# Performance work log

Measured on AMD Instinct MI355X. Metric: run time of the kernel, lower is better.

The kernel has to match this reference:

```python
import jax, jax.numpy as jnp
import numpy as np

B, H, N = 2, 4, 8192
K = 32       # sub_size
TEMP = 2.0   # temperature for the soft permutation indicator


def setup_inputs() -> dict:
    key = jax.random.key(0)
    ranking = jax.random.normal(key, (B, H, N, 1), dtype=jnp.float32)
    return {"ranking": ranking, "i": 0, "j": N}


@jax.custom_vjp
def hsigmoid(x):
    # Hard step indicator (x > 0) with straight-through gradient (CoCN Hsigmoid)
    return (x > 0).astype(x.dtype)

def _hs_fwd(x):
    return hsigmoid(x), None

def _hs_bwd(res, g):
    return (g,)

hsigmoid.defvjp(_hs_fwd, _hs_bwd)


def _windows(x, n, k):
    # circular pad last dim by k-1, then unfold into sliding windows of size k
    xp = jnp.concatenate([x, x[..., :k - 1]], axis=-1)
    idx = jnp.arange(n)[:, None] + jnp.arange(k)[None, :]   # (n, k)
    return xp[..., idx]                                      # (..., n, k)


def reference(ranking, i, j):
    b, h, n = ranking.shape[:3]
    k = K
    r = ranking[..., 0]                                      # (b,h,n)
    order = jnp.argsort(r, axis=2, stable=True)              # (b,h,n) stable sort indices
    r_sorted = jnp.take_along_axis(r, order, axis=2)

    val_win = _windows(r_sorted, n, k)                       # (b,h,n,k)
    idx_win = _windows(order.astype(jnp.float32), n, k).astype(jnp.int32)

    # scatter windows back to original node order == gather by inverse permutation
    inv = jnp.argsort(order, axis=2)                         # (b,h,n)
    val_win = jnp.take_along_axis(val_win, inv[..., None], axis=2)
    idx_win = jnp.take_along_axis(idx_win, inv[..., None], axis=2)

    # within each window, sort by original node index (stable), reorder values alike
    k_order = jnp.argsort(idx_win, axis=-1, stable=True)
    sorted_idx = jnp.take_along_axis(idx_win, k_order, axis=-1)
    val_win = jnp.take_along_axis(val_win, k_order, axis=-1)

    # slice node window [i, i+j)
    val_win = val_win[:, :, i:i + j]                         # (b,h,j,k)
    sorted_idx = sorted_idx[:, :, i:i + j]

    # (b,j,h,k) -> (b*j, h, k, 1)
    x = jnp.transpose(val_win, (0, 2, 1, 3)).reshape(-1, h, k, 1)
    rel = x - jnp.swapaxes(x, -1, -2)                        # (b*j,h,k,k)
    tie_bias = jnp.triu((rel == 0).astype(jnp.float32), 1)   # break ties above diagonal
    rel = rel + tie_bias
    uni = hsigmoid(jax.nn.relu(rel))                         # 1 where strictly greater
    rank = jnp.sum(uni, axis=-2, keepdims=True)              # (b*j,h,1,k)

    ind = jnp.arange(k, dtype=jnp.float32)[:, None] - rank   # (b*j,h,k,k)
    ind = jnp.where(ind < 0, ind + k, ind)
    perm = jnp.exp(-ind * TEMP)
    return perm, sorted_idx
```

## Files before the change

kernel.cpp:

```cpp
#include <hip/hip_runtime.h>
#include <stdint.h>

#define B_ 2
#define H_ 4
#define N_ 8192
#define K_ 32
#define ROWS 8
#define NTOT (ROWS * N_)
#define PERM_ELEMS ((size_t)B_ * N_ * H_ * K_ * K_)

__global__ __launch_bounds__(256) void pack_keys(const float* __restrict__ ranking,
                                                 uint64_t* __restrict__ keys,
                                                 int* __restrict__ rank) {
    const int g = blockIdx.x * 256 + threadIdx.x;
    uint32_t u = __float_as_uint(ranking[g]);
    u = (u & 0x80000000u) ? ~u : (u | 0x80000000u);
    keys[g] = ((uint64_t)u << 13) | (uint32_t)(g & (N_ - 1));
    rank[g] = 0;
}

#define JT 1024
#define IT 2048
#define EPT 8

__global__ __launch_bounds__(256) void rank_count(const uint64_t* __restrict__ keys,
                                                  int* __restrict__ rank) {
    __shared__ uint64_t jk[JT];
    const int blk = blockIdx.x;
    const int jt  = blk & 7;
    const int it  = (blk >> 3) & 3;
    const int row = blk >> 5;
    const uint64_t* rk = keys + (size_t)row * N_;

    for (int j = threadIdx.x; j < JT; j += 256)
        jk[j] = rk[jt * JT + j];

    uint64_t my[EPT];
    const int ibase = it * IT + threadIdx.x;
    #pragma unroll
    for (int e = 0; e < EPT; ++e) my[e] = rk[ibase + e * 256];
    __syncthreads();

    int cnt[EPT] = {0, 0, 0, 0, 0, 0, 0, 0};
    for (int j = 0; j < JT; j += 2) {
        const uint64_t k0 = jk[j];
        const uint64_t k1 = jk[j + 1];
        #pragma unroll
        for (int e = 0; e < EPT; ++e) {
            cnt[e] += (k0 < my[e]);
            cnt[e] += (k1 < my[e]);
        }
    }
    #pragma unroll
    for (int e = 0; e < EPT; ++e)
        atomicAdd(&rank[(size_t)row * N_ + ibase + e * 256], cnt[e]);
}

__global__ __launch_bounds__(256) void scatter_sorted(const float* __restrict__ ranking,
                                                      const int* __restrict__ rank,
                                                      int2* __restrict__ vid,
                                                      int* __restrict__ inv) {
    const int g = blockIdx.x * 256 + threadIdx.x;
    const int row = g >> 13;
    const int s = rank[g];
    inv[g] = s;
    vid[(size_t)row * N_ + s] = make_int2(__float_as_int(ranking[g]), g & (N_ - 1));
}

__global__ __launch_bounds__(256) void windows_kernel(
    const int2* __restrict__ vid,
    const int* __restrict__ inv,
    float* __restrict__ perm_out,
    float* __restrict__ idx_out)
{
    __shared__ float etabN[K_];
    __shared__ float etabP[K_];
    __shared__ uint64_t wk[8][K_];
    __shared__ float2 cinfo[8][K_ + 1];
    __shared__ float idf[8][K_];

    const int tid = threadIdx.x;
    if (tid < K_) {
        etabN[tid] = expf(-2.0f * (float)tid);
        etabP[tid] = expf(2.0f * (float)tid);
    }

    const int wave = tid >> 6;
    const int lane = tid & 63;
    const int half = lane >> 5;
    const int m    = lane & 31;
    const int ws   = wave * 2 + half;

    const int w   = blockIdx.x * 8 + ws;
    const int row = w >> 13;
    const int n   = w & (N_ - 1);

    const int t = inv[(size_t)row * N_ + n];
    int g = t + m; if (g >= N_) g -= N_;
    const int2 vi = vid[(size_t)row * N_ + g];
    const int id = vi.y;
    uint32_t u = (uint32_t)vi.x;
    u = (u & 0x80000000u) ? ~u : (u | 0x80000000u);
    const int rid = (N_ - 1) - id;
    const uint64_t key2 = ((uint64_t)u << 13) | (uint32_t)rid;

    wk[ws][m] = key2;
    __syncthreads();

    int rank = 0, pos = 0;
    #pragma unroll
    for (int p = 0; p < K_; ++p) {
        const uint64_t kp = wk[ws][p];
        rank += (kp > key2);
        pos  += ((int)((uint32_t)kp & (uint32_t)(N_ - 1)) > rid);
    }

    cinfo[ws][pos] = make_float2(etabP[rank], __int_as_float(rank));
    idf[ws][pos]   = (float)id;
    __syncthreads();

    idx_out[((size_t)row * N_ + n) * K_ + m] = idf[ws][m];

    const int b = row >> 2;
    const int h = row & 3;
    float4* pout = (float4*)(perm_out + (((size_t)b * N_ + n) * H_ + h) * (K_ * K_));
    const float E64C = 1.6038108e-28f;

    #pragma unroll
    for (int q = 0; q < 8; ++q) {
        const int f4 = q * 32 + m;
        const int mm = f4 >> 3;
        const int j0 = (f4 & 7) * 4;
        const float a = etabN[mm];
        const float2 c0 = cinfo[ws][j0 + 0];
        const float2 c1 = cinfo[ws][j0 + 1];
        const float2 c2 = cinfo[ws][j0 + 2];
        const float2 c3 = cinfo[ws][j0 + 3];
        float4 val;
        val.x = a * c0.x * (mm < __float_as_int(c0.y) ? E64C : 1.0f);
        val.y = a * c1.x * (mm < __float_as_int(c1.y) ? E64C : 1.0f);
        val.z = a * c2.x * (mm < __float_as_int(c2.y) ? E64C : 1.0f);
        val.w = a * c3.x * (mm < __float_as_int(c3.y) ? E64C : 1.0f);
        pout[f4] = val;
    }
}

extern "C" void kernel_launch(void* const* d_in, const int* in_sizes, int n_in,
                              void* d_out, int out_size, void* d_ws, size_t ws_size,
                              hipStream_t stream) {
    const float* ranking = (const float*)d_in[0];

    char* ws = (char*)d_ws;
    uint64_t* keys = (uint64_t*)ws;
    int*      rank = (int*)(ws + 512 * 1024);
    int2*     vid  = (int2*)(ws + 768 * 1024);
    int*      inv  = (int*)(ws + 1280 * 1024);

    float* perm_out = (float*)d_out;
    float* idx_out  = perm_out + PERM_ELEMS;

    hipLaunchKernelGGL(pack_keys, dim3(NTOT / 256), dim3(256), 0, stream,
                       ranking, keys, rank);
    hipLaunchKernelGGL(rank_count, dim3(256), dim3(256), 0, stream,
                       keys, rank);
    hipLaunchKernelGGL(scatter_sorted, dim3(NTOT / 256), dim3(256), 0, stream,
                       ranking, rank, vid, inv);
    hipLaunchKernelGGL(windows_kernel, dim3((ROWS * N_) / 8), dim3(256), 0, stream,
                       vid, inv, perm_out, idx_out);
}
```

Measured before the change: 318.2 us.

## Fuse rank counting with scatter and hoist window-loop loads

Merges the tiled rank-count kernel (which used atomics) and the scatter kernel into one kernel. Each block loads a full row of keys into shared memory and each thread computes its full rank directly, which removes the atomic adds, the rank buffer zeroing and one launch. Each thread now does 8192 comparisons for a single element, so the block count stays at 256 while the per-thread serial work and the shared-memory footprint (64KB) go up. In the windows kernel the cinfo loads are hoisted out of the output loop and the exp table lookup is replaced by a running multiplication, which may introduce small floating-point rounding differences.

```diff
diff --git a/kernel.cpp b/kernel.cpp
--- a/kernel.cpp
+++ b/kernel.cpp
@@ -10,61 +10,46 @@
 #define PERM_ELEMS ((size_t)B_ * N_ * H_ * K_ * K_)
 
 __global__ __launch_bounds__(256) void pack_keys(const float* __restrict__ ranking,
-                                                 uint64_t* __restrict__ keys,
-                                                 int* __restrict__ rank) {
+                                                 uint64_t* __restrict__ keys) {
     const int g = blockIdx.x * 256 + threadIdx.x;
     uint32_t u = __float_as_uint(ranking[g]);
     u = (u & 0x80000000u) ? ~u : (u | 0x80000000u);
     keys[g] = ((uint64_t)u << 13) | (uint32_t)(g & (N_ - 1));
-    rank[g] = 0;
 }
 
-#define JT 1024
-#define IT 2048
-#define EPT 8
-
-__global__ __launch_bounds__(256) void rank_count(const uint64_t* __restrict__ keys,
-                                                  int* __restrict__ rank) {
-    __shared__ uint64_t jk[JT];
-    const int blk = blockIdx.x;
-    const int jt  = blk & 7;
-    const int it  = (blk >> 3) & 3;
-    const int row = blk >> 5;
+__global__ __launch_bounds__(256) void rank_scatter(const uint64_t* __restrict__ keys,
+                                                    const float* __restrict__ ranking,
+                                                    int2* __restrict__ vid,
+                                                    int* __restrict__ inv) {
+    __shared__ uint64_t jk[N_];
+    const int row   = blockIdx.x >> 5;
+    const int itile = blockIdx.x & 31;
     const uint64_t* rk = keys + (size_t)row * N_;
 
-    for (int j = threadIdx.x; j < JT; j += 256)
-        jk[j] = rk[jt * JT + j];
+    for (int j = threadIdx.x; j < N_; j += 256)
+        jk[j] = rk[j];
 
-    uint64_t my[EPT];
-    const int ibase = it * IT + threadIdx.x;
-    #pragma unroll
-    for (int e = 0; e < EPT; ++e) my[e] = rk[ibase + e * 256];
+    const int i  = itile * 256 + threadIdx.x;
+    const uint64_t my = rk[i];
     __syncthreads();
 
-    int cnt[EPT] = {0, 0, 0, 0, 0, 0, 0, 0};
-    for (int j = 0; j < JT; j += 2) {
-        const uint64_t k0 = jk[j];
-        const uint64_t k1 = jk[j + 1];
+    int c0 = 0, c1 = 0, c2 = 0, c3 = 0;
+    for (int j = 0; j < N_; j += 16) {
+        uint64_t k[16];
         #pragma unroll
-        for (int e = 0; e < EPT; ++e) {
-            cnt[e] += (k0 < my[e]);
-            cnt[e] += (k1 < my[e]);
+        for (int t = 0; t < 16; ++t) k[t] = jk[j + t];
+        #pragma unroll
+        for (int t = 0; t < 4; ++t) {
+            c0 += (k[t * 4 + 0] < my);
+            c1 += (k[t * 4 + 1] < my);
+            c2 += (k[t * 4 + 2] < my);
+            c3 += (k[t * 4 + 3] < my);
         }
     }
-    #pragma unroll
-    for (int e = 0; e < EPT; ++e)
-        atomicAdd(&rank[(size_t)row * N_ + ibase + e * 256], cnt[e]);
-}
-
-__global__ __launch_bounds__(256) void scatter_sorted(const float* __restrict__ ranking,
-                                                      const int* __restrict__ rank,
-                                                      int2* __restrict__ vid,
-                                                      int* __restrict__ inv) {
-    const int g = blockIdx.x * 256 + threadIdx.x;
-    const int row = g >> 13;
-    const int s = rank[g];
+    const int s = c0 + c1 + c2 + c3;
+    const int g = row * N_ + i;
     inv[g] = s;
-    vid[(size_t)row * N_ + s] = make_int2(__float_as_int(ranking[g]), g & (N_ - 1));
+    vid[(size_t)row * N_ + s] = make_int2(__float_as_int(ranking[g]), i);
 }
 
 __global__ __launch_bounds__(256) void windows_kernel(
@@ -73,17 +58,13 @@
     float* __restrict__ perm_out,
     float* __restrict__ idx_out)
 {
-    __shared__ float etabN[K_];
     __shared__ float etabP[K_];
     __shared__ uint64_t wk[8][K_];
     __shared__ float2 cinfo[8][K_ + 1];
     __shared__ float idf[8][K_];
 
     const int tid = threadIdx.x;
-    if (tid < K_) {
-        etabN[tid] = expf(-2.0f * (float)tid);
-        etabP[tid] = expf(2.0f * (float)tid);
-    }
+    if (tid < K_) etabP[tid] = expf(2.0f * (float)tid);
 
     const int wave = tid >> 6;
     const int lane = tid & 63;
@@ -124,24 +105,31 @@
     const int b = row >> 2;
     const int h = row & 3;
     float4* pout = (float4*)(perm_out + (((size_t)b * N_ + n) * H_ + h) * (K_ * K_));
+
+    const int j0 = (m & 7) * 4;
+    const float2 c0 = cinfo[ws][j0 + 0];
+    const float2 c1 = cinfo[ws][j0 + 1];
+    const float2 c2 = cinfo[ws][j0 + 2];
+    const float2 c3 = cinfo[ws][j0 + 3];
+    const int r0 = __float_as_int(c0.y), r1 = __float_as_int(c1.y);
+    const int r2 = __float_as_int(c2.y), r3 = __float_as_int(c3.y);
+
+    const int mbase = m >> 3;
+    float a = (mbase & 1 ? 0.13533528f : 1.0f) * (mbase & 2 ? 0.018315639f : 1.0f);
+    const float EM8 = 3.3546262e-4f;
     const float E64C = 1.6038108e-28f;
+    int mm = mbase;
 
     #pragma unroll
     for (int q = 0; q < 8; ++q) {
-        const int f4 = q * 32 + m;
-        const int mm = f4 >> 3;
-        const int j0 = (f4 & 7) * 4;
-        const float a = etabN[mm];
-        const float2 c0 = cinfo[ws][j0 + 0];
-        const float2 c1 = cinfo[ws][j0 + 1];
-        const float2 c2 = cinfo[ws][j0 + 2];
-        const float2 c3 = cinfo[ws][j0 + 3];
         float4 val;
-        val.x = a * c0.x * (mm < __float_as_int(c0.y) ? E64C : 1.0f);
-        val.y = a * c1.x * (mm < __float_as_int(c1.y) ? E64C : 1.0f);
-        val.z = a * c2.x * (mm < __float_as_int(c2.y) ? E64C : 1.0f);
-        val.w = a * c3.x * (mm < __float_as_int(c3.y) ? E64C : 1.0f);
-        pout[f4] = val;
+        val.x = a * c0.x * (mm < r0 ? E64C : 1.0f);
+        val.y = a * c1.x * (mm < r1 ? E64C : 1.0f);
+        val.z = a * c2.x * (mm < r2 ? E64C : 1.0f);
+        val.w = a * c3.x * (mm < r3 ? E64C : 1.0f);
+        pout[q * 32 + m] = val;
+        a *= EM8;
+        mm += 4;
     }
 }
 
@@ -152,19 +140,16 @@
 
     char* ws = (char*)d_ws;
     uint64_t* keys = (uint64_t*)ws;
-    int*      rank = (int*)(ws + 512 * 1024);
-    int2*     vid  = (int2*)(ws + 768 * 1024);
-    int*      inv  = (int*)(ws + 1280 * 1024);
+    int2*     vid  = (int2*)(ws + 512 * 1024);
+    int*      inv  = (int*)(ws + 1024 * 1024);
 
     float* perm_out = (float*)d_out;
     float* idx_out  = perm_out + PERM_ELEMS;
 
     hipLaunchKernelGGL(pack_keys, dim3(NTOT / 256), dim3(256), 0, stream,
-                       ranking, keys, rank);
-    hipLaunchKernelGGL(rank_count, dim3(256), dim3(256), 0, stream,
-                       keys, rank);
-    hipLaunchKernelGGL(scatter_sorted, dim3(NTOT / 256), dim3(256), 0, stream,
-                       ranking, rank, vid, inv);
+                       ranking, keys);
+    hipLaunchKernelGGL(rank_scatter, dim3(256), dim3(256), 0, stream,
+                       keys, ranking, vid, inv);
     hipLaunchKernelGGL(windows_kernel, dim3((ROWS * N_) / 8), dim3(256), 0, stream,
                        vid, inv, perm_out, idx_out);
 }
```

Measured after the change: 333.6 us. 4.8% more time.
